# Kernel tuning notes

Measured on AMD Instinct MI355X. Metric: run time of the kernel, lower is better.

The kernel has to match this reference:

```python
import jax, jax.numpy as jnp
import numpy as np

D_MODEL = 1024
N_HEADS = 16
D_K = D_MODEL // N_HEADS
LN_EPS = 1e-5
NEG = -1e9


def setup_inputs() -> dict:
    key = jax.random.key(0)
    ks = jax.random.split(key, 12)
    B, S = 4, 2048
    s = 1.0 / np.sqrt(D_MODEL)
    # causal mask (1 = keep, 0 = masked)
    causal = jnp.tril(jnp.ones((S, S), dtype=jnp.int32))
    mask = jnp.broadcast_to(causal[None, None], (B, 1, S, S))
    return {
        "Q": jax.random.normal(ks[0], (B, S, D_MODEL), jnp.float32),
        "K": jax.random.normal(ks[1], (B, S, D_MODEL), jnp.float32),
        "V": jax.random.normal(ks[2], (B, S, D_MODEL), jnp.float32),
        "mask": mask,
        "Wq": jax.random.normal(ks[3], (D_MODEL, D_MODEL), jnp.float32) * s,
        "bq": jnp.zeros((D_MODEL,), jnp.float32),
        "Wk": jax.random.normal(ks[4], (D_MODEL, D_MODEL), jnp.float32) * s,
        "bk": jnp.zeros((D_MODEL,), jnp.float32),
        "Wv": jax.random.normal(ks[5], (D_MODEL, D_MODEL), jnp.float32) * s,
        "bv": jnp.zeros((D_MODEL,), jnp.float32),
        "Wo": jax.random.normal(ks[6], (D_MODEL, D_MODEL), jnp.float32) * s,
        "bo": jnp.zeros((D_MODEL,), jnp.float32),
        "ln_gamma": jnp.ones((D_MODEL,), jnp.float32),
        "ln_beta": jnp.zeros((D_MODEL,), jnp.float32),
    }


def _split_heads(x, B, S):
    # (B,S,D) -> (B,H,S,d_k)
    return x.reshape(B, S, N_HEADS, D_K).transpose(0, 2, 1, 3)


def reference(Q, K, V, mask, Wq, bq, Wk, bk, Wv, bv, Wo, bo, ln_gamma, ln_beta):
    B, S, _ = Q.shape
    residual = Q
    q = _split_heads(Q @ Wq + bq, B, S)
    k = _split_heads(K @ Wk + bk, B, S)
    v = _split_heads(V @ Wv + bv, B, S)
    scores = jnp.einsum("bhqd,bhkd->bhqk", q, k) / np.sqrt(D_K).astype(np.float32)
    scores = jnp.where(mask == 0, jnp.float32(NEG), scores)
    attn = jax.nn.softmax(scores, axis=-1)  # dropout p=0 -> identity
    ctx = jnp.einsum("bhqk,bhkd->bhqd", attn, v)
    ctx = ctx.transpose(0, 2, 1, 3).reshape(B, S, D_MODEL)
    out = ctx @ Wo + bo
    x = out + residual
    mu = jnp.mean(x, axis=-1, keepdims=True)
    var = jnp.mean(jnp.square(x - mu), axis=-1, keepdims=True)
    y = (x - mu) * jax.lax.rsqrt(var + LN_EPS) * ln_gamma + ln_beta
    return (y, attn)
```

## Files before the change

kernel.cpp:

```cpp
#include <hip/hip_runtime.h>

#define D_MODEL 1024
#define NH 16
#define DKH 64
#define SEQ 2048
#define BATCH 4
#define ROWS (BATCH*SEQ)

typedef _Float16 f16;
typedef _Float16 f16x4 __attribute__((ext_vector_type(4)));
typedef _Float16 f16x8 __attribute__((ext_vector_type(8)));
typedef float f32x4 __attribute__((ext_vector_type(4)));

#define MFMA16(a,b,c) __builtin_amdgcn_mfma_f32_16x16x32_f16((a),(b),(c),0,0,0)

__device__ __forceinline__ void gload16(const void* g, void* l) {
  __builtin_amdgcn_global_load_lds((const __attribute__((address_space(1))) void*)g,
                                   (__attribute__((address_space(3))) void*)l,
                                   16, 0, 0);
}


__global__ __launch_bounds__(256) void cvt_x_kernel(const float* __restrict__ Q,
    const float* __restrict__ K, const float* __restrict__ V, f16* __restrict__ dst)
{
  const float* src = (blockIdx.z==0) ? Q : (blockIdx.z==1) ? K : V;
  f16* d = dst + (size_t)blockIdx.z * ((size_t)ROWS*D_MODEL);
  size_t i = (size_t)blockIdx.x*256 + threadIdx.x;
  float4 v = ((const float4*)src)[i];
  f16x4 o; o[0]=(f16)v.x; o[1]=(f16)v.y; o[2]=(f16)v.z; o[3]=(f16)v.w;
  ((f16x4*)d)[i] = o;
}

__global__ __launch_bounds__(256) void cvt_w_kernel(const float* __restrict__ Wq,
    const float* __restrict__ Wk, const float* __restrict__ Wv, const float* __restrict__ Wo,
    f16* __restrict__ dst)
{
  const float* W = (blockIdx.z==0)?Wq:(blockIdx.z==1)?Wk:(blockIdx.z==2)?Wv:Wo;
  f16* d = dst + (size_t)blockIdx.z * ((size_t)D_MODEL*D_MODEL);
  int idx = blockIdx.x*256 + threadIdx.x;
  int k = idx>>10, n = idx&1023;
  d[(size_t)n*D_MODEL + k] = (f16)W[idx];
}


__global__ __launch_bounds__(256) void gemm128(
    const f16* __restrict__ Abase, const f16* __restrict__ WTbase,
    const float* __restrict__ bias0, const float* __restrict__ bias1, const float* __restrict__ bias2,
    f16* __restrict__ out0, f16* __restrict__ out1, f16* __restrict__ out2,
    const float* __restrict__ resid, float* __restrict__ xout, int modeBase)
{
  __shared__ f16 Al[128*32];
  __shared__ f16 Bl[128*32];
  const int t = threadIdx.x, w = t>>6, l = t&63;
  const int mode = modeBase + blockIdx.z;
  const f16* A = (modeBase==0) ? Abase + (size_t)blockIdx.z*((size_t)ROWS*D_MODEL) : Abase;
  const f16* WT = WTbase + (size_t)mode * ((size_t)D_MODEL*D_MODEL);
  const float* bias = (mode==0)?bias0:(mode==1)?bias1:(mode==2)?bias2:bias0;
  const int bn = blockIdx.x, bm = blockIdx.y;
  const int wm = w>>1, wn = w&1;
  const int lr = l>>2, lc = l&3, fr = l&15, fg = l>>4;
  f32x4 acc[4][4] = {};
  const char* Ab = (const char*)(A  + (size_t)bm*128*D_MODEL);
  const char* Bb = (const char*)(WT + (size_t)bn*128*D_MODEL);

  for (int kt=0; kt<32; ++kt) {
    __syncthreads();
    #pragma unroll
    for (int cc=0; cc<2; ++cc) {
      int r0 = w*32 + cc*16;
      gload16(Ab + (size_t)(r0+lr)*2048 + kt*64 + lc*16, (char*)Al + r0*64);
      gload16(Bb + (size_t)(r0+lr)*2048 + kt*64 + lc*16, (char*)Bl + r0*64);
    }
    __syncthreads();
    f16x8 a[4], b[4];
    #pragma unroll
    for (int i=0;i<4;++i) a[i] = *(const f16x8*)(Al + (wm*64+i*16+fr)*32 + fg*8);
    #pragma unroll
    for (int j=0;j<4;++j) b[j] = *(const f16x8*)(Bl + (wn*64+j*16+fr)*32 + fg*8);
    #pragma unroll
    for (int i=0;i<4;++i)
      #pragma unroll
      for (int j=0;j<4;++j)
        acc[i][j] = MFMA16(a[i], b[j], acc[i][j]);
  }

  #pragma unroll
  for (int j=0;j<4;++j) {
    int col = bn*128 + wn*64 + j*16 + fr;
    float bz = bias[col];
    #pragma unroll
    for (int i=0;i<4;++i) {
      int row0 = bm*128 + wm*64 + i*16 + fg*4;
      f32x4 v = acc[i][j];
      if (mode==0) {
        int hh = col>>6, dk = col&63;
        #pragma unroll
        for (int r=0;r<4;++r) {
          int row = row0+r; int b_ = row>>11, s = row&(SEQ-1);
          out0[((size_t)(b_*NH+hh)*SEQ + s)*DKH + dk] = (f16)((v[r]+bz)*0.125f);
        }
      } else if (mode==1) {
        int hh = col>>6, dk = col&63;
        #pragma unroll
        for (int r=0;r<4;++r) {
          int row = row0+r; int b_ = row>>11, s = row&(SEQ-1);
          out1[((size_t)(b_*NH+hh)*SEQ + s)*DKH + dk] = (f16)(v[r]+bz);
        }
      } else if (mode==2) {
        int hh = col>>6, dk = col&63;
        int b_ = row0>>11, s0 = row0&(SEQ-1);
        f16x4 pk;
        #pragma unroll
        for (int r=0;r<4;++r) pk[r] = (f16)(v[r]+bz);
        *(f16x4*)(out2 + ((size_t)(b_*NH+hh)*DKH + dk)*SEQ + s0) = pk;
      } else {
        #pragma unroll
        for (int r=0;r<4;++r) {
          size_t o = (size_t)(row0+r)*D_MODEL + col;
          xout[o] = v[r] + bz + resid[o];
        }
      }
    }
  }
}


__global__ __launch_bounds__(256) void attn_kernel(
    const f16* __restrict__ qws, const f16* __restrict__ kws, const f16* __restrict__ vTws,
    float* __restrict__ attn, f16* __restrict__ ctx)
{
  __shared__ f16 ql[2][128*32];
  __shared__ f16 kl[2][128*32];
  __shared__ f16 vl[4][64*32];
  __shared__ f16 el[4][128*32];
  const int t = threadIdx.x, w = t>>6, l = t&63;
  const int qt = 15 - (int)blockIdx.x;
  const int bh = blockIdx.y;
  const int lr=l>>2, lc=l&3, fr=l&15, fg=l>>4;
  const f16* qp = qws + ((size_t)bh*SEQ + (size_t)qt*128)*DKH;
  const f16* kp = kws + (size_t)bh*SEQ*DKH;
  const f16* vp = vTws + (size_t)bh*DKH*SEQ;
  float* ap = attn + ((size_t)bh*SEQ + (size_t)qt*128)*SEQ;

  for (int kt2=qt+1; kt2<16; ++kt2) {
    float4 z = make_float4(0.f,0.f,0.f,0.f);
    #pragma unroll
    for (int i=0;i<16;++i) {
      int idx = t + i*256;
      int row = idx>>5, c4 = idx&31;
      ((float4*)(ap + (size_t)row*SEQ + kt2*128))[c4] = z;
    }
  }

  #pragma unroll
  for (int kc=0;kc<2;++kc)
    #pragma unroll
    for (int cc=0;cc<2;++cc) {
      int r0 = w*32 + cc*16;
      gload16((const char*)qp + (size_t)(r0+lr)*128 + kc*64 + lc*16, (char*)ql[kc] + r0*64);
    }

  float psum[2][4] = {};
  for (int kt=0; kt<=qt; ++kt) {
    __syncthreads();
    #pragma unroll
    for (int kc=0;kc<2;++kc)
      #pragma unroll
      for (int cc=0;cc<2;++cc) {
        int r0 = w*32 + cc*16;
        gload16((const char*)kp + (size_t)(kt*128 + r0 + lr)*128 + kc*64 + lc*16, (char*)kl[kc] + r0*64);
      }
    __syncthreads();
    f32x4 sc[2][8] = {};
    #pragma unroll
    for (int kc=0;kc<2;++kc) {
      f16x8 a0 = *(const f16x8*)(ql[kc] + (w*32+fr)*32 + fg*8);
      f16x8 a1 = *(const f16x8*)(ql[kc] + (w*32+16+fr)*32 + fg*8);
      #pragma unroll
      for (int j=0;j<8;++j) {
        f16x8 bb = *(const f16x8*)(kl[kc] + (j*16+fr)*32 + fg*8);
        sc[0][j] = MFMA16(a0, bb, sc[0][j]);
        sc[1][j] = MFMA16(a1, bb, sc[1][j]);
      }
    }
    #pragma unroll
    for (int i=0;i<2;++i)
      #pragma unroll
      for (int j=0;j<8;++j) {
        int colg = kt*128 + j*16 + fr;
        #pragma unroll
        for (int r=0;r<4;++r) {
          int rowg = qt*128 + w*32 + i*16 + fg*4 + r;
          if (colg <= rowg) psum[i][r] += __expf(sc[i][j][r]);
        }
      }
  }
  #pragma unroll
  for (int m=1;m<16;m<<=1)
    #pragma unroll
    for (int i=0;i<2;++i)
      #pragma unroll
      for (int r=0;r<4;++r)
        psum[i][r] += __shfl_xor(psum[i][r], m, 64);
  float rinv[2][4];
  #pragma unroll
  for (int i=0;i<2;++i)
    #pragma unroll
    for (int r=0;r<4;++r) rinv[i][r] = 1.f/psum[i][r];

  f32x4 av[2][4] = {};
  for (int kt=0; kt<=qt; ++kt) {
    __syncthreads();
    #pragma unroll
    for (int kc=0;kc<2;++kc)
      #pragma unroll
      for (int cc=0;cc<2;++cc) {
        int r0 = w*32 + cc*16;
        gload16((const char*)kp + (size_t)(kt*128 + r0 + lr)*128 + kc*64 + lc*16, (char*)kl[kc] + r0*64);
      }
    #pragma unroll
    for (int cc=0;cc<4;++cc) {
      int dk0 = cc*16;
      gload16((const char*)vp + ((size_t)(dk0+lr)*SEQ + (size_t)kt*128 + w*32)*2 + lc*16, (char*)vl[w] + dk0*64);
    }
    __syncthreads();
    f32x4 sc[2][8] = {};
    #pragma unroll
    for (int kc=0;kc<2;++kc) {
      f16x8 a0 = *(const f16x8*)(ql[kc] + (w*32+fr)*32 + fg*8);
      f16x8 a1 = *(const f16x8*)(ql[kc] + (w*32+16+fr)*32 + fg*8);
      #pragma unroll
      for (int j=0;j<8;++j) {
        f16x8 bb = *(const f16x8*)(kl[kc] + (j*16+fr)*32 + fg*8);
        sc[0][j] = MFMA16(a0, bb, sc[0][j]);
        sc[1][j] = MFMA16(a1, bb, sc[1][j]);
      }
    }
    #pragma unroll
    for (int i=0;i<2;++i)
      #pragma unroll
      for (int j=0;j<8;++j) {
        int colg = kt*128 + j*16 + fr;
        int ch = j>>1, wcol = (j&1)*16 + fr;
        #pragma unroll
        for (int r=0;r<4;++r) {
          int rowl = w*32 + i*16 + fg*4 + r;
          int rowg = qt*128 + rowl;
          float e = (colg<=rowg) ? __expf(sc[i][j][r]) * rinv[i][r] : 0.f;
          ap[(size_t)rowl*SEQ + colg] = e;
          el[ch][rowl*32 + wcol] = (f16)e;
        }
      }
    #pragma unroll
    for (int c=0;c<4;++c) {
      f16x8 a0 = *(const f16x8*)(el[c] + (w*32+fr)*32 + fg*8);
      f16x8 a1 = *(const f16x8*)(el[c] + (w*32+16+fr)*32 + fg*8);
      #pragma unroll
      for (int j=0;j<4;++j) {
        f16x8 bb = *(const f16x8*)(vl[c] + (j*16+fr)*32 + fg*8);
        av[0][j] = MFMA16(a0, bb, av[0][j]);
        av[1][j] = MFMA16(a1, bb, av[1][j]);
      }
    }
  }
  const int b_ = bh>>4, hh = bh&15;
  #pragma unroll
  for (int i=0;i<2;++i)
    #pragma unroll
    for (int j=0;j<4;++j) {
      int dk = j*16+fr;
      #pragma unroll
      for (int r=0;r<4;++r) {
        int s = qt*128 + w*32 + i*16 + fg*4 + r;
        ctx[((size_t)b_*SEQ + s)*D_MODEL + hh*DKH + dk] = (f16)av[i][j][r];
      }
    }
}


__global__ __launch_bounds__(256) void ln_kernel(const float* __restrict__ x,
    const float* __restrict__ gamma, const float* __restrict__ beta, float* __restrict__ y)
{
  __shared__ float red[4];
  __shared__ float red2[4];
  const int t = threadIdx.x, w = t>>6, l = t&63;
  const size_t row = blockIdx.x;
  float4 v = ((const float4*)(x + row*D_MODEL))[t];
  float s = v.x+v.y+v.z+v.w;
  #pragma unroll
  for (int m=1;m<64;m<<=1) s += __shfl_xor(s, m, 64);
  if (l==0) red[w] = s;
  __syncthreads();
  float mu = (red[0]+red[1]+red[2]+red[3]) * (1.f/D_MODEL);
  float dx=v.x-mu, dy=v.y-mu, dz=v.z-mu, dw=v.w-mu;
  float q = dx*dx+dy*dy+dz*dz+dw*dw;
  #pragma unroll
  for (int m=1;m<64;m<<=1) q += __shfl_xor(q, m, 64);
  if (l==0) red2[w] = q;
  __syncthreads();
  float var = (red2[0]+red2[1]+red2[2]+red2[3]) * (1.f/D_MODEL);
  float rs = rsqrtf(var + 1e-5f);
  float4 g  = ((const float4*)gamma)[t];
  float4 bb = ((const float4*)beta)[t];
  float4 o;
  o.x = dx*rs*g.x + bb.x;
  o.y = dy*rs*g.y + bb.y;
  o.z = dz*rs*g.z + bb.z;
  o.w = dw*rs*g.w + bb.w;
  ((float4*)(y + row*D_MODEL))[t] = o;
}


extern "C" void kernel_launch(void* const* d_in, const int* in_sizes, int n_in,
                              void* d_out, int out_size, void* d_ws, size_t ws_size,
                              hipStream_t stream)
{
  const float* Q  = (const float*)d_in[0];
  const float* K  = (const float*)d_in[1];
  const float* V  = (const float*)d_in[2];
  const float* Wq = (const float*)d_in[4];
  const float* bq = (const float*)d_in[5];
  const float* Wk = (const float*)d_in[6];
  const float* bk = (const float*)d_in[7];
  const float* Wv = (const float*)d_in[8];
  const float* bv = (const float*)d_in[9];
  const float* Wo = (const float*)d_in[10];
  const float* bo = (const float*)d_in[11];
  const float* gam= (const float*)d_in[12];
  const float* bet= (const float*)d_in[13];

  float* y    = (float*)d_out;
  float* attn = y + (size_t)ROWS*D_MODEL;

  char* ws = (char*)d_ws;
  const size_t SZ = (size_t)ROWS*D_MODEL*sizeof(f16);
  f16* Xb    = (f16*)ws;
  f16* ctx   = (f16*)ws;
  float* xb  = (float*)(ws + SZ);
  f16* WT    = (f16*)(ws + 3*SZ);
  f16* qws   = (f16*)(ws + 3*SZ + ((size_t)4*D_MODEL*D_MODEL*sizeof(f16)));
  f16* kws   = (f16*)((char*)qws + SZ);
  f16* vT    = (f16*)((char*)kws + SZ);

  cvt_x_kernel<<<dim3(8192,1,3), 256, 0, stream>>>(Q, K, V, Xb);
  cvt_w_kernel<<<dim3(4096,1,4), 256, 0, stream>>>(Wq, Wk, Wv, Wo, WT);
  gemm128<<<dim3(8,64,3), 256, 0, stream>>>(Xb, WT, bq, bk, bv, qws, kws, vT, nullptr, nullptr, 0);
  attn_kernel<<<dim3(16,64), 256, 0, stream>>>(qws, kws, vT, attn, ctx);
  gemm128<<<dim3(8,64,1), 256, 0, stream>>>(ctx, WT, bo, bo, bo, nullptr, nullptr, nullptr, Q, xb, 3);
  ln_kernel<<<8192, 256, 0, stream>>>(xb, gam, bet, y);
}
```

Before: 529.3 us.

## Restructure attention to read K/V from registers, remap blocks across XCDs

The attention kernel drops the shared-memory staging of Q, K and V and the block barriers. It loads fragments straight from global memory into registers and swaps the MFMA operand order so each lane owns whole rows, which makes row sums and vectorised stores simpler. The probability tile now goes through a per-wave swizzled LDS buffer. Attention output and zero-fill use nontemporal vector stores. Both GEMM and attention grids are flattened and remapped so neighbouring tiles land on the same XCD, for better L2 locality. The trade-off is more redundant global/L2 reads of K and V per wave in exchange for no barriers.

```diff
diff --git a/kernel.cpp b/kernel.cpp
--- a/kernel.cpp
+++ b/kernel.cpp
@@ -53,11 +53,15 @@
   __shared__ f16 Al[128*32];
   __shared__ f16 Bl[128*32];
   const int t = threadIdx.x, w = t>>6, l = t&63;
-  const int mode = modeBase + blockIdx.z;
-  const f16* A = (modeBase==0) ? Abase + (size_t)blockIdx.z*((size_t)ROWS*D_MODEL) : Abase;
+  const int nwg = (int)gridDim.x;
+  const int wg = ((int)blockIdx.x & 7) * (nwg >> 3) + ((int)blockIdx.x >> 3);
+  const int z  = wg >> 9;
+  const int r2 = wg & 511;
+  const int bm = r2 >> 3, bn = r2 & 7;
+  const int mode = modeBase + z;
+  const f16* A = (modeBase==0) ? Abase + (size_t)z*((size_t)ROWS*D_MODEL) : Abase;
   const f16* WT = WTbase + (size_t)mode * ((size_t)D_MODEL*D_MODEL);
   const float* bias = (mode==0)?bias0:(mode==1)?bias1:(mode==2)?bias2:bias0;
-  const int bn = blockIdx.x, bm = blockIdx.y;
   const int wm = w>>1, wn = w&1;
   const int lr = l>>2, lc = l&3, fr = l&15, fg = l>>4;
   f32x4 acc[4][4] = {};
@@ -130,152 +134,128 @@
     const f16* __restrict__ qws, const f16* __restrict__ kws, const f16* __restrict__ vTws,
     float* __restrict__ attn, f16* __restrict__ ctx)
 {
-  __shared__ f16 ql[2][128*32];
-  __shared__ f16 kl[2][128*32];
-  __shared__ f16 vl[4][64*32];
-  __shared__ f16 el[4][128*32];
+  __shared__ f16 el[4][32*128];
   const int t = threadIdx.x, w = t>>6, l = t&63;
-  const int qt = 15 - (int)blockIdx.x;
-  const int bh = blockIdx.y;
-  const int lr=l>>2, lc=l&3, fr=l&15, fg=l>>4;
+  const int wg = ((int)blockIdx.x & 7)*128 + ((int)blockIdx.x >> 3);
+  const int bh = wg >> 4;
+  const int qt = 15 - (wg & 15);
+  const int fr = l & 15, fg = l >> 4;
   const f16* qp = qws + ((size_t)bh*SEQ + (size_t)qt*128)*DKH;
   const f16* kp = kws + (size_t)bh*SEQ*DKH;
   const f16* vp = vTws + (size_t)bh*DKH*SEQ;
   float* ap = attn + ((size_t)bh*SEQ + (size_t)qt*128)*SEQ;
-
-  for (int kt2=qt+1; kt2<16; ++kt2) {
-    float4 z = make_float4(0.f,0.f,0.f,0.f);
-    #pragma unroll
-    for (int i=0;i<16;++i) {
-      int idx = t + i*256;
-      int row = idx>>5, c4 = idx&31;
-      ((float4*)(ap + (size_t)row*SEQ + kt2*128))[c4] = z;
-    }
-  }
-
-  #pragma unroll
-  for (int kc=0;kc<2;++kc)
-    #pragma unroll
-    for (int cc=0;cc<2;++cc) {
-      int r0 = w*32 + cc*16;
-      gload16((const char*)qp + (size_t)(r0+lr)*128 + kc*64 + lc*16, (char*)ql[kc] + r0*64);
-    }
-
-  float psum[2][4] = {};
+  f16* elw = (f16*)&el[w][0];
+
+  for (int kt2 = qt+1; kt2 < 16; ++kt2) {
+    f32x4 z4 = {0.f,0.f,0.f,0.f};
+    #pragma unroll
+    for (int i2=0;i2<16;++i2) {
+      int idx = t + i2*256;
+      int row = idx >> 5, c4 = idx & 31;
+      __builtin_nontemporal_store(z4, (f32x4*)(ap + (size_t)row*SEQ + (size_t)kt2*128 + c4*4));
+    }
+  }
+
+  f16x8 qf[2][2];
+  #pragma unroll
+  for (int i=0;i<2;++i)
+    #pragma unroll
+    for (int kc=0;kc<2;++kc)
+      qf[i][kc] = *(const f16x8*)(qp + (w*32 + i*16 + fr)*DKH + kc*32 + fg*8);
+
+#define COMPUTE_SC(sc, ktv) do { \
+    const f16* kb = kp + (size_t)(ktv)*128*DKH; \
+    _Pragma("unroll") \
+    for (int j=0;j<8;++j) { \
+      _Pragma("unroll") \
+      for (int kc=0;kc<2;++kc) { \
+        f16x8 kf = *(const f16x8*)(kb + (j*16+fr)*DKH + kc*32 + fg*8); \
+        sc[0][j] = MFMA16(kf, qf[0][kc], sc[0][j]); \
+        sc[1][j] = MFMA16(kf, qf[1][kc], sc[1][j]); \
+      } \
+    } \
+  } while(0)
+
+  float psum[2] = {0.f, 0.f};
   for (int kt=0; kt<=qt; ++kt) {
-    __syncthreads();
-    #pragma unroll
-    for (int kc=0;kc<2;++kc)
-      #pragma unroll
-      for (int cc=0;cc<2;++cc) {
-        int r0 = w*32 + cc*16;
-        gload16((const char*)kp + (size_t)(kt*128 + r0 + lr)*128 + kc*64 + lc*16, (char*)kl[kc] + r0*64);
+    f32x4 sc[2][8] = {};
+    COMPUTE_SC(sc, kt);
+    if (kt == qt) {
+      #pragma unroll
+      for (int i=0;i<2;++i) {
+        int rloc = w*32 + i*16 + fr;
+        #pragma unroll
+        for (int j=0;j<8;++j)
+          #pragma unroll
+          for (int r=0;r<4;++r) {
+            int cloc = j*16 + fg*4 + r;
+            if (cloc <= rloc) psum[i] += __expf(sc[i][j][r]);
+          }
       }
-    __syncthreads();
+    } else {
+      #pragma unroll
+      for (int i=0;i<2;++i)
+        #pragma unroll
+        for (int j=0;j<8;++j)
+          #pragma unroll
+          for (int r=0;r<4;++r) psum[i] += __expf(sc[i][j][r]);
+    }
+  }
+  #pragma unroll
+  for (int m=16; m<64; m<<=1) {
+    psum[0] += __shfl_xor(psum[0], m, 64);
+    psum[1] += __shfl_xor(psum[1], m, 64);
+  }
+  float rinv[2] = {1.f/psum[0], 1.f/psum[1]};
+
+  f32x4 av[2][4] = {};
+  const int swzx = (fr & 7) << 2;
+  for (int kt=0; kt<=qt; ++kt) {
     f32x4 sc[2][8] = {};
-    #pragma unroll
-    for (int kc=0;kc<2;++kc) {
-      f16x8 a0 = *(const f16x8*)(ql[kc] + (w*32+fr)*32 + fg*8);
-      f16x8 a1 = *(const f16x8*)(ql[kc] + (w*32+16+fr)*32 + fg*8);
+    COMPUTE_SC(sc, kt);
+    const bool diag = (kt == qt);
+    #pragma unroll
+    for (int i=0;i<2;++i) {
+      const int rloc = w*32 + i*16 + fr;
       #pragma unroll
       for (int j=0;j<8;++j) {
-        f16x8 bb = *(const f16x8*)(kl[kc] + (j*16+fr)*32 + fg*8);
-        sc[0][j] = MFMA16(a0, bb, sc[0][j]);
-        sc[1][j] = MFMA16(a1, bb, sc[1][j]);
+        f32x4 ev; f16x4 ef;
+        #pragma unroll
+        for (int r=0;r<4;++r) {
+          int cloc = j*16 + fg*4 + r;
+          float e = (diag && cloc > rloc) ? 0.f : __expf(sc[i][j][r]) * rinv[i];
+          ev[r] = e; ef[r] = (f16)e;
+        }
+        __builtin_nontemporal_store(ev, (f32x4*)(ap + (size_t)rloc*SEQ + (size_t)kt*128 + j*16 + fg*4));
+        *(f16x4*)(elw + (i*16+fr)*128 + (((j*4+fg) ^ swzx) << 2)) = ef;
       }
     }
     #pragma unroll
-    for (int i=0;i<2;++i)
-      #pragma unroll
-      for (int j=0;j<8;++j) {
-        int colg = kt*128 + j*16 + fr;
-        #pragma unroll
-        for (int r=0;r<4;++r) {
-          int rowg = qt*128 + w*32 + i*16 + fg*4 + r;
-          if (colg <= rowg) psum[i][r] += __expf(sc[i][j][r]);
-        }
+    for (int c=0;c<4;++c) {
+      f16x8 pf0 = *(const f16x8*)(elw + (fr)*128    + (((c*8+fg*2) ^ swzx) << 2));
+      f16x8 pf1 = *(const f16x8*)(elw + (16+fr)*128 + (((c*8+fg*2) ^ swzx) << 2));
+      #pragma unroll
+      for (int j2=0;j2<4;++j2) {
+        f16x8 vf = *(const f16x8*)(vp + (j2*16+fr)*SEQ + kt*128 + c*32 + fg*8);
+        av[0][j2] = MFMA16(vf, pf0, av[0][j2]);
+        av[1][j2] = MFMA16(vf, pf1, av[1][j2]);
       }
-  }
-  #pragma unroll
-  for (int m=1;m<16;m<<=1)
-    #pragma unroll
-    for (int i=0;i<2;++i)
-      #pragma unroll
-      for (int r=0;r<4;++r)
-        psum[i][r] += __shfl_xor(psum[i][r], m, 64);
-  float rinv[2][4];
-  #pragma unroll
-  for (int i=0;i<2;++i)
-    #pragma unroll
-    for (int r=0;r<4;++r) rinv[i][r] = 1.f/psum[i][r];
-
-  f32x4 av[2][4] = {};
-  for (int kt=0; kt<=qt; ++kt) {
-    __syncthreads();
-    #pragma unroll
-    for (int kc=0;kc<2;++kc)
-      #pragma unroll
-      for (int cc=0;cc<2;++cc) {
-        int r0 = w*32 + cc*16;
-        gload16((const char*)kp + (size_t)(kt*128 + r0 + lr)*128 + kc*64 + lc*16, (char*)kl[kc] + r0*64);
-      }
-    #pragma unroll
-    for (int cc=0;cc<4;++cc) {
-      int dk0 = cc*16;
-      gload16((const char*)vp + ((size_t)(dk0+lr)*SEQ + (size_t)kt*128 + w*32)*2 + lc*16, (char*)vl[w] + dk0*64);
-    }
-    __syncthreads();
-    f32x4 sc[2][8] = {};
-    #pragma unroll
-    for (int kc=0;kc<2;++kc) {
-      f16x8 a0 = *(const f16x8*)(ql[kc] + (w*32+fr)*32 + fg*8);
-      f16x8 a1 = *(const f16x8*)(ql[kc] + (w*32+16+fr)*32 + fg*8);
-      #pragma unroll
-      for (int j=0;j<8;++j) {
-        f16x8 bb = *(const f16x8*)(kl[kc] + (j*16+fr)*32 + fg*8);
-        sc[0][j] = MFMA16(a0, bb, sc[0][j]);
-        sc[1][j] = MFMA16(a1, bb, sc[1][j]);
-      }
-    }
-    #pragma unroll
-    for (int i=0;i<2;++i)
-      #pragma unroll
-      for (int j=0;j<8;++j) {
-        int colg = kt*128 + j*16 + fr;
-        int ch = j>>1, wcol = (j&1)*16 + fr;
-        #pragma unroll
-        for (int r=0;r<4;++r) {
-          int rowl = w*32 + i*16 + fg*4 + r;
-          int rowg = qt*128 + rowl;
-          float e = (colg<=rowg) ? __expf(sc[i][j][r]) * rinv[i][r] : 0.f;
-          ap[(size_t)rowl*SEQ + colg] = e;
-          el[ch][rowl*32 + wcol] = (f16)e;
-        }
-      }
-    #pragma unroll
-    for (int c=0;c<4;++c) {
-      f16x8 a0 = *(const f16x8*)(el[c] + (w*32+fr)*32 + fg*8);
-      f16x8 a1 = *(const f16x8*)(el[c] + (w*32+16+fr)*32 + fg*8);
-      #pragma unroll
-      for (int j=0;j<4;++j) {
-        f16x8 bb = *(const f16x8*)(vl[c] + (j*16+fr)*32 + fg*8);
-        av[0][j] = MFMA16(a0, bb, av[0][j]);
-        av[1][j] = MFMA16(a1, bb, av[1][j]);
-      }
-    }
-  }
-  const int b_ = bh>>4, hh = bh&15;
-  #pragma unroll
-  for (int i=0;i<2;++i)
-    #pragma unroll
-    for (int j=0;j<4;++j) {
-      int dk = j*16+fr;
-      #pragma unroll
-      for (int r=0;r<4;++r) {
-        int s = qt*128 + w*32 + i*16 + fg*4 + r;
-        ctx[((size_t)b_*SEQ + s)*D_MODEL + hh*DKH + dk] = (f16)av[i][j][r];
-      }
-    }
+    }
+  }
+
+  const int b_ = bh >> 4, hh = bh & 15;
+  #pragma unroll
+  for (int i=0;i<2;++i) {
+    size_t rowoff = ((size_t)b_*SEQ + (size_t)qt*128 + w*32 + i*16 + fr) * D_MODEL + hh*DKH;
+    #pragma unroll
+    for (int j2=0;j2<4;++j2) {
+      f16x4 pk;
+      #pragma unroll
+      for (int r=0;r<4;++r) pk[r] = (f16)av[i][j2][r];
+      *(f16x4*)(ctx + rowoff + j2*16 + fg*4) = pk;
+    }
+  }
+#undef COMPUTE_SC
 }
 
 
@@ -345,8 +325,8 @@
 
   cvt_x_kernel<<<dim3(8192,1,3), 256, 0, stream>>>(Q, K, V, Xb);
   cvt_w_kernel<<<dim3(4096,1,4), 256, 0, stream>>>(Wq, Wk, Wv, Wo, WT);
-  gemm128<<<dim3(8,64,3), 256, 0, stream>>>(Xb, WT, bq, bk, bv, qws, kws, vT, nullptr, nullptr, 0);
-  attn_kernel<<<dim3(16,64), 256, 0, stream>>>(qws, kws, vT, attn, ctx);
-  gemm128<<<dim3(8,64,1), 256, 0, stream>>>(ctx, WT, bo, bo, bo, nullptr, nullptr, nullptr, Q, xb, 3);
+  gemm128<<<1536, 256, 0, stream>>>(Xb, WT, bq, bk, bv, qws, kws, vT, nullptr, nullptr, 0);
+  attn_kernel<<<1024, 256, 0, stream>>>(qws, kws, vT, attn, ctx);
+  gemm128<<<512, 256, 0, stream>>>(ctx, WT, bo, bo, bo, nullptr, nullptr, nullptr, Q, xb, 3);
   ln_kernel<<<8192, 256, 0, stream>>>(xb, gam, bet, y);
 }
```

New measurement: 528.3 us. About the same (-0.2%).
